# Kernel tuning notes

Measured on AMD Instinct MI355X. Metric: run time of the kernel, lower is better.

Reference implementation:

```python
import jax, jax.numpy as jnp
import numpy as np

NEG_SLOPE = 0.2
TAU_MRF = 1.0
N_NODES = 100000
PROJ_DIM = 128
GAT_DIM = 64
N_EDGES = 1000000


def setup_inputs() -> dict:
    key = jax.random.key(0)
    ks = jax.random.split(key, 8)
    z_beh = jax.random.normal(ks[0], (N_NODES, PROJ_DIM), dtype=jnp.float32)
    z_pref = jax.random.normal(ks[1], (N_NODES, PROJ_DIM), dtype=jnp.float32)
    edge_index = jax.random.randint(ks[2], (2, N_EDGES), 0, N_NODES, dtype=jnp.int64)
    # xavier_uniform for [GAT_DIM, PROJ_DIM] linear weights
    lim_w = float(np.sqrt(6.0 / (PROJ_DIM + GAT_DIM)))
    W_b = jax.random.uniform(ks[3], (GAT_DIM, PROJ_DIM), minval=-lim_w, maxval=lim_w, dtype=jnp.float32)
    W_p = jax.random.uniform(ks[4], (GAT_DIM, PROJ_DIM), minval=-lim_w, maxval=lim_w, dtype=jnp.float32)
    # xavier_uniform on view(1, 2D): fan_in=1? torch treats [1, 2D] -> fan_in=2D, fan_out=1
    lim_a = float(np.sqrt(6.0 / (1 + 2 * GAT_DIM)))
    a_b = jax.random.uniform(ks[5], (2 * GAT_DIM,), minval=-lim_a, maxval=lim_a, dtype=jnp.float32)
    a_p = jax.random.uniform(ks[6], (2 * GAT_DIM,), minval=-lim_a, maxval=lim_a, dtype=jnp.float32)
    gamma_b = jnp.zeros((), dtype=jnp.float32)
    gamma_p = jnp.zeros((), dtype=jnp.float32)
    return {"z_beh": z_beh, "z_pref": z_pref, "W_b": W_b, "W_p": W_p,
            "a_b": a_b, "a_p": a_p, "gamma_b": gamma_b, "gamma_p": gamma_p,
            "edge_index_undirected": edge_index}


def _sym_score(h, a, src, dst, neg_slope):
    # e_ij = leaky_relu((cat[h_src, h_dst]) . a). Split a to avoid materializing
    # the [E, 2D] concat: dot each node once, then gather scalars per edge.
    D = h.shape[-1]
    si = h @ a[:D]   # [N] contribution of left slot
    sj = h @ a[D:]   # [N] contribution of right slot
    e_ij = jax.nn.leaky_relu(si[src] + sj[dst], negative_slope=neg_slope)
    e_ji = jax.nn.leaky_relu(si[dst] + sj[src], negative_slope=neg_slope)
    return 0.5 * (e_ij + e_ji)


def reference(z_beh, z_pref, W_b, W_p, a_b, a_p, gamma_b, gamma_p, edge_index_undirected):
    src = edge_index_undirected[0]
    dst = edge_index_undirected[1]
    h_b = z_beh @ W_b.T   # [N, D]
    h_p = z_pref @ W_p.T  # [N, D]
    s_b = _sym_score(h_b, a_b, src, dst, NEG_SLOPE)  # [E]
    s_p = _sym_score(h_p, a_p, src, dst, NEG_SLOPE)  # [E]
    w = jax.nn.softmax(jnp.stack([gamma_b, gamma_p]))
    s = w[0] * s_b + w[1] * s_p
    alpha_ij = jax.nn.sigmoid(s / TAU_MRF)
    return alpha_ij
```

## Files before the change

### kernel.cpp

```cpp
#include <hip/hip_runtime.h>
#include <hip/hip_bf16.h>

#define NEG_SLOPE 0.2f

__global__ void compute_v_kernel(const float* __restrict__ W_b,
                                 const float* __restrict__ W_p,
                                 const float* __restrict__ a_b,
                                 const float* __restrict__ a_p,
                                 float* __restrict__ v) {
    const int t = threadIdx.x;
    const int p = t & 127;
    const int ch = t >> 7;
    const float* W = ch ? W_p : W_b;
    const float* a = ch ? a_p : a_b;
    float acc1 = 0.f, acc2 = 0.f;
    #pragma unroll
    for (int d = 0; d < 64; ++d) {
        const float w = W[d * 128 + p];
        acc1 += w * a[d];
        acc2 += w * a[64 + d];
    }
    v[(2 * ch + 0) * 128 + p] = acc1;
    v[(2 * ch + 1) * 128 + p] = acc2;
}

__global__ void node_scores_kernel(const float4* __restrict__ zb4,
                                   const float4* __restrict__ zp4,
                                   const float* __restrict__ v,
                                   float4* __restrict__ tab,
                                   int n_nodes) {
    const int lane = threadIdx.x & 63;
    const int h    = lane >> 5;
    const int c    = lane & 31;
    const int wave   = (blockIdx.x * blockDim.x + threadIdx.x) >> 6;
    const int nwaves = (gridDim.x * blockDim.x) >> 6;
    const int npairs = (n_nodes + 1) >> 1;

    const float4 v1b = *reinterpret_cast<const float4*>(v + 0 * 128 + 4 * c);
    const float4 v2b = *reinterpret_cast<const float4*>(v + 1 * 128 + 4 * c);
    const float4 v1p = *reinterpret_cast<const float4*>(v + 2 * 128 + 4 * c);
    const float4 v2p = *reinterpret_cast<const float4*>(v + 3 * 128 + 4 * c);

    for (int pr = wave; pr < npairs; pr += nwaves) {
        int node = 2 * pr + h;
        const int valid = node < n_nodes;
        if (!valid) node = n_nodes - 1;
        const size_t base = (size_t)node * 32 + c;
        const float4 zb = zb4[base];
        const float4 zp = zp4[base];
        float sib = zb.x * v1b.x + zb.y * v1b.y + zb.z * v1b.z + zb.w * v1b.w;
        float sjb = zb.x * v2b.x + zb.y * v2b.y + zb.z * v2b.z + zb.w * v2b.w;
        float sip = zp.x * v1p.x + zp.y * v1p.y + zp.z * v1p.z + zp.w * v1p.w;
        float sjp = zp.x * v2p.x + zp.y * v2p.y + zp.z * v2p.z + zp.w * v2p.w;
        #pragma unroll
        for (int off = 16; off > 0; off >>= 1) {
            sib += __shfl_xor(sib, off);
            sjb += __shfl_xor(sjb, off);
            sip += __shfl_xor(sip, off);
            sjp += __shfl_xor(sjp, off);
        }
        if (c == 0 && valid) {
            tab[node] = make_float4(sib, sjb, sip, sjp);
        }
    }
}

__device__ __forceinline__ float lrelu(float x) {
    return x >= 0.f ? x : NEG_SLOPE * x;
}

__device__ __forceinline__ float edge_score(const float4 ts, const float4 td,
                                            float w0, float w1) {
    const float sb = 0.5f * (lrelu(ts.x + td.y) + lrelu(td.x + ts.y));
    const float sp = 0.5f * (lrelu(ts.z + td.w) + lrelu(td.z + ts.w));
    const float sc = w0 * sb + w1 * sp;
    return 1.f / (1.f + __expf(-sc));
}

__global__ void edge_scores_kernel(const int2* __restrict__ src2,
                                   const int2* __restrict__ dst2,
                                   const float4* __restrict__ tab,
                                   const float* __restrict__ gamma_b,
                                   const float* __restrict__ gamma_p,
                                   float2* __restrict__ out2,
                                   int n_pairs) {
    const float gb = *gamma_b;
    const float gp = *gamma_p;
    const float w0 = 1.f / (1.f + __expf(gp - gb));
    const float w1 = 1.f - w0;

    const int stride = gridDim.x * blockDim.x;
    for (int i = blockIdx.x * blockDim.x + threadIdx.x; i < n_pairs; i += stride) {
        const int2 s = src2[i];
        const int2 d = dst2[i];
        const float4 ts0 = tab[s.x];
        const float4 td0 = tab[d.x];
        const float4 ts1 = tab[s.y];
        const float4 td1 = tab[d.y];
        float2 r;
        r.x = edge_score(ts0, td0, w0, w1);
        r.y = edge_score(ts1, td1, w0, w1);
        out2[i] = r;
    }
}

extern "C" void kernel_launch(void* const* d_in, const int* in_sizes, int n_in,
                              void* d_out, int out_size, void* d_ws, size_t ws_size,
                              hipStream_t stream) {
    const float* z_beh  = (const float*)d_in[0];
    const float* z_pref = (const float*)d_in[1];
    const float* W_b    = (const float*)d_in[2];
    const float* W_p    = (const float*)d_in[3];
    const float* a_b    = (const float*)d_in[4];
    const float* a_p    = (const float*)d_in[5];
    const float* g_b    = (const float*)d_in[6];
    const float* g_p    = (const float*)d_in[7];
    const int*   ei     = (const int*)d_in[8];

    const int n_nodes = in_sizes[0] / 128;
    const int n_edges = in_sizes[8] / 2;

    float*  v   = (float*)d_ws;
    float4* tab = (float4*)((char*)d_ws + 2048);

    compute_v_kernel<<<1, 256, 0, stream>>>(W_b, W_p, a_b, a_p, v);

    node_scores_kernel<<<2048, 256, 0, stream>>>(
        (const float4*)z_beh, (const float4*)z_pref, v, tab, n_nodes);

    const int n_epairs = n_edges / 2;
    const int eblocks  = (n_epairs + 255) / 256;
    edge_scores_kernel<<<(eblocks < 2048 ? eblocks : 2048), 256, 0, stream>>>(
        (const int2*)ei, (const int2*)(ei + n_edges), tab, g_b, g_p,
        (float2*)d_out, n_epairs);
}
```

Baseline: 39.19 us.

## Fuse projection-vector kernel into node scores, vectorize edge kernel to four edges

Removes the separate single-block kernel that computes the projected attention vectors. Every node-score block now recomputes them into shared memory, which saves one launch and one serialization point. The edge kernel now handles four edges per thread with 128-bit index loads and stores, and the streaming z, index and output traffic uses nontemporal loads and stores. The cost is redundant W·a work in each of the 2048 blocks, plus a tail loop for edge counts not divisible by four.

```diff
diff --git a/kernel.cpp b/kernel.cpp
--- a/kernel.cpp
+++ b/kernel.cpp
@@ -3,51 +3,56 @@
 
 #define NEG_SLOPE 0.2f
 
-__global__ void compute_v_kernel(const float* __restrict__ W_b,
-                                 const float* __restrict__ W_p,
-                                 const float* __restrict__ a_b,
-                                 const float* __restrict__ a_p,
-                                 float* __restrict__ v) {
+typedef float f32x4 __attribute__((ext_vector_type(4)));
+typedef int   i32x4 __attribute__((ext_vector_type(4)));
+
+__global__ void __launch_bounds__(256) node_scores_kernel(
+        const float*  __restrict__ W_b,
+        const float*  __restrict__ W_p,
+        const float*  __restrict__ a_b,
+        const float*  __restrict__ a_p,
+        const f32x4*  __restrict__ zb4,
+        const f32x4*  __restrict__ zp4,
+        f32x4*        __restrict__ tab,
+        int n_nodes) {
+    __shared__ float vsh[4][128];
+
     const int t = threadIdx.x;
-    const int p = t & 127;
-    const int ch = t >> 7;
-    const float* W = ch ? W_p : W_b;
-    const float* a = ch ? a_p : a_b;
-    float acc1 = 0.f, acc2 = 0.f;
-    #pragma unroll
-    for (int d = 0; d < 64; ++d) {
-        const float w = W[d * 128 + p];
-        acc1 += w * a[d];
-        acc2 += w * a[64 + d];
+    {
+        const int p    = t & 127;
+        const int half = t >> 7;
+        const float* ab = a_b + 64 * half;
+        const float* ap = a_p + 64 * half;
+        float accb = 0.f, accp = 0.f;
+        #pragma unroll
+        for (int d = 0; d < 64; ++d) {
+            accb += W_b[d * 128 + p] * ab[d];
+            accp += W_p[d * 128 + p] * ap[d];
+        }
+        vsh[half][p]     = accb;
+        vsh[2 + half][p] = accp;
     }
-    v[(2 * ch + 0) * 128 + p] = acc1;
-    v[(2 * ch + 1) * 128 + p] = acc2;
-}
+    __syncthreads();
 
-__global__ void node_scores_kernel(const float4* __restrict__ zb4,
-                                   const float4* __restrict__ zp4,
-                                   const float* __restrict__ v,
-                                   float4* __restrict__ tab,
-                                   int n_nodes) {
-    const int lane = threadIdx.x & 63;
+    const int lane = t & 63;
     const int h    = lane >> 5;
     const int c    = lane & 31;
-    const int wave   = (blockIdx.x * blockDim.x + threadIdx.x) >> 6;
+    const int wave   = (blockIdx.x * blockDim.x + t) >> 6;
     const int nwaves = (gridDim.x * blockDim.x) >> 6;
     const int npairs = (n_nodes + 1) >> 1;
 
-    const float4 v1b = *reinterpret_cast<const float4*>(v + 0 * 128 + 4 * c);
-    const float4 v2b = *reinterpret_cast<const float4*>(v + 1 * 128 + 4 * c);
-    const float4 v1p = *reinterpret_cast<const float4*>(v + 2 * 128 + 4 * c);
-    const float4 v2p = *reinterpret_cast<const float4*>(v + 3 * 128 + 4 * c);
+    const f32x4 v1b = *reinterpret_cast<const f32x4*>(&vsh[0][4 * c]);
+    const f32x4 v2b = *reinterpret_cast<const f32x4*>(&vsh[1][4 * c]);
+    const f32x4 v1p = *reinterpret_cast<const f32x4*>(&vsh[2][4 * c]);
+    const f32x4 v2p = *reinterpret_cast<const f32x4*>(&vsh[3][4 * c]);
 
     for (int pr = wave; pr < npairs; pr += nwaves) {
         int node = 2 * pr + h;
         const int valid = node < n_nodes;
         if (!valid) node = n_nodes - 1;
         const size_t base = (size_t)node * 32 + c;
-        const float4 zb = zb4[base];
-        const float4 zp = zp4[base];
+        const f32x4 zb = __builtin_nontemporal_load(&zb4[base]);
+        const f32x4 zp = __builtin_nontemporal_load(&zp4[base]);
         float sib = zb.x * v1b.x + zb.y * v1b.y + zb.z * v1b.z + zb.w * v1b.w;
         float sjb = zb.x * v2b.x + zb.y * v2b.y + zb.z * v2b.z + zb.w * v2b.w;
         float sip = zp.x * v1p.x + zp.y * v1p.y + zp.z * v1p.z + zp.w * v1p.w;
@@ -60,7 +65,9 @@
             sjp += __shfl_xor(sjp, off);
         }
         if (c == 0 && valid) {
-            tab[node] = make_float4(sib, sjb, sip, sjp);
+            f32x4 r;
+            r.x = sib; r.y = sjb; r.z = sip; r.w = sjp;
+            tab[node] = r;
         }
     }
 }
@@ -69,7 +76,7 @@
     return x >= 0.f ? x : NEG_SLOPE * x;
 }
 
-__device__ __forceinline__ float edge_score(const float4 ts, const float4 td,
+__device__ __forceinline__ float edge_score(const f32x4 ts, const f32x4 td,
                                             float w0, float w1) {
     const float sb = 0.5f * (lrelu(ts.x + td.y) + lrelu(td.x + ts.y));
     const float sp = 0.5f * (lrelu(ts.z + td.w) + lrelu(td.z + ts.w));
@@ -77,30 +84,40 @@
     return 1.f / (1.f + __expf(-sc));
 }
 
-__global__ void edge_scores_kernel(const int2* __restrict__ src2,
-                                   const int2* __restrict__ dst2,
-                                   const float4* __restrict__ tab,
-                                   const float* __restrict__ gamma_b,
-                                   const float* __restrict__ gamma_p,
-                                   float2* __restrict__ out2,
-                                   int n_pairs) {
+__global__ void __launch_bounds__(256) edge_scores_kernel(
+        const int*    __restrict__ src,
+        const int*    __restrict__ dst,
+        const f32x4*  __restrict__ tab,
+        const float*  __restrict__ gamma_b,
+        const float*  __restrict__ gamma_p,
+        float*        __restrict__ out,
+        int n_edges) {
     const float gb = *gamma_b;
     const float gp = *gamma_p;
     const float w0 = 1.f / (1.f + __expf(gp - gb));
     const float w1 = 1.f - w0;
 
-    const int stride = gridDim.x * blockDim.x;
-    for (int i = blockIdx.x * blockDim.x + threadIdx.x; i < n_pairs; i += stride) {
-        const int2 s = src2[i];
-        const int2 d = dst2[i];
-        const float4 ts0 = tab[s.x];
-        const float4 td0 = tab[d.x];
-        const float4 ts1 = tab[s.y];
-        const float4 td1 = tab[d.y];
-        float2 r;
-        r.x = edge_score(ts0, td0, w0, w1);
-        r.y = edge_score(ts1, td1, w0, w1);
-        out2[i] = r;
+    const int n_quads = n_edges >> 2;
+    const int stride  = gridDim.x * blockDim.x;
+    const int gid     = blockIdx.x * blockDim.x + threadIdx.x;
+
+    const i32x4* src4 = (const i32x4*)src;
+    const i32x4* dst4 = (const i32x4*)dst;
+    f32x4*       out4 = (f32x4*)out;
+
+    for (int i = gid; i < n_quads; i += stride) {
+        const i32x4 s = __builtin_nontemporal_load(&src4[i]);
+        const i32x4 d = __builtin_nontemporal_load(&dst4[i]);
+        f32x4 r;
+        r.x = edge_score(tab[s.x], tab[d.x], w0, w1);
+        r.y = edge_score(tab[s.y], tab[d.y], w0, w1);
+        r.z = edge_score(tab[s.z], tab[d.z], w0, w1);
+        r.w = edge_score(tab[s.w], tab[d.w], w0, w1);
+        __builtin_nontemporal_store(r, &out4[i]);
+    }
+    const int tail_base = n_quads << 2;
+    for (int e = tail_base + gid; e < n_edges; e += stride) {
+        out[e] = edge_score(tab[src[e]], tab[dst[e]], w0, w1);
     }
 }
 
@@ -120,17 +137,16 @@
     const int n_nodes = in_sizes[0] / 128;
     const int n_edges = in_sizes[8] / 2;
 
-    float*  v   = (float*)d_ws;
-    float4* tab = (float4*)((char*)d_ws + 2048);
-
-    compute_v_kernel<<<1, 256, 0, stream>>>(W_b, W_p, a_b, a_p, v);
+    f32x4* tab = (f32x4*)d_ws;
 
     node_scores_kernel<<<2048, 256, 0, stream>>>(
-        (const float4*)z_beh, (const float4*)z_pref, v, tab, n_nodes);
+        W_b, W_p, a_b, a_p,
+        (const f32x4*)z_beh, (const f32x4*)z_pref, tab, n_nodes);
 
-    const int n_epairs = n_edges / 2;
-    const int eblocks  = (n_epairs + 255) / 256;
-    edge_scores_kernel<<<(eblocks < 2048 ? eblocks : 2048), 256, 0, stream>>>(
-        (const int2*)ei, (const int2*)(ei + n_edges), tab, g_b, g_p,
-        (float2*)d_out, n_epairs);
+    const int n_quads = n_edges >> 2;
+    int eblocks = (n_quads + 255) / 256;
+    if (eblocks > 2048) eblocks = 2048;
+    if (eblocks < 1) eblocks = 1;
+    edge_scores_kernel<<<eblocks, 256, 0, stream>>>(
+        ei, ei + n_edges, tab, g_b, g_p, (float*)d_out, n_edges);
 }
```

Result: slower. 47.17 us (+20.4%).
